# Kernel tuning notes

Hardware: AMD Instinct MI355X
Metric: run time of the kernel (lower is better)

Reference implementation:

```python
import jax, jax.numpy as jnp
import numpy as np

D = 128      # dim_hidden
L = 8        # topological levels (level 0 = primary inputs)
M = 32768    # nodes per level
N = L * M
G = 5        # gate types: maj/not/and/or/xor -> 5 param sets
F = 2        # fan-in per gate node


def setup_inputs() -> dict:
    key = jax.random.key(0)
    ks = jax.random.split(key, 18)
    p = lambda k, sh: jax.random.normal(k, sh, jnp.float32) * 0.05
    return {
        's': jax.random.normal(ks[0], (N, D), jnp.float32),
        't': jax.random.normal(ks[1], (N, D), jnp.float32),
        'gate': jax.random.randint(ks[2], (N,), 0, G, jnp.int32),
        'fanin': jax.random.randint(ks[3], (L - 1, M, F), 0, M, jnp.int32),
        'hs_W': p(ks[4], (2 * D, D)), 'hs_b': p(ks[5], (D,)),
        'aggr_W1': p(ks[6], (G, 2 * D, D)), 'aggr_b1': p(ks[7], (G, D)),
        'aggr_W2': p(ks[8], (G, D, D)), 'aggr_b2': p(ks[9], (G, D)),
        'aggr_W3': p(ks[10], (G, D, D)), 'aggr_b3': p(ks[11], (G, D)),
        'gru_Wi': p(ks[12], (G, D, 3 * D)), 'gru_Wh': p(ks[13], (G, D, 3 * D)),
        'gru_bi': p(ks[14], (G, 3 * D)), 'gru_bh': p(ks[15], (G, 3 * D)),
    }


def _forward(s, t, gate, fanin, hs_W, hs_b, aggr_W1, aggr_b1, aggr_W2, aggr_b2,
             aggr_W3, aggr_b3, gru_Wi, gru_Wh, gru_bi, gru_bh):
    hs = jnp.concatenate([s, t], -1) @ hs_W + hs_b          # [N,D]
    hf = jnp.zeros((N, D), hs.dtype)                        # functional state, zero-init
    for lvl in range(1, L):                                 # level-synchronous sweep
        lo = lvl * M
        g_l = gate[lo:lo + M]                               # [M] gate type of dst nodes
        oh = jax.nn.one_hot(g_l, G, dtype=hs.dtype)         # [M,G] gate selector
        src = (lvl - 1) * M + fanin[lvl - 1]                # [M,F] global fan-in indices
        src_state = jnp.concatenate([hs[src], hf[src]], -1)  # [M,F,2D] node_state gather
        # per-gate-type edge MLP (TFMlpAggr): 3-layer MLP on source states, sum over fan-in
        h1 = jax.nn.relu(jnp.einsum('mfc,gcd->gmfd', src_state, aggr_W1) + aggr_b1[:, None, None, :])
        h2 = jax.nn.relu(jnp.einsum('gmfd,gde->gmfe', h1, aggr_W2) + aggr_b2[:, None, None, :])
        m = jnp.einsum('gmfe,gek->gmfk', h2, aggr_W3) + aggr_b3[:, None, None, :]
        msg = jnp.einsum('gmd,mg->md', m.sum(axis=2), oh)   # [M,D] select own gate's aggr
        # per-gate-type GRU update of hf (torch GRU math, seq_len=1)
        h = hf[lo:lo + M]                                   # [M,D]
        gi = jnp.einsum('md,gdk->gmk', msg, gru_Wi) + gru_bi[:, None, :]  # [G,M,3D]
        gh = jnp.einsum('md,gdk->gmk', h, gru_Wh) + gru_bh[:, None, :]
        r = jax.nn.sigmoid(gi[..., :D] + gh[..., :D])
        z = jax.nn.sigmoid(gi[..., D:2 * D] + gh[..., D:2 * D])
        n = jnp.tanh(gi[..., 2 * D:] + r * gh[..., 2 * D:])
        h_new = jnp.einsum('gmd,mg->md', (1.0 - z) * n + z * h[None], oh)
        hf = hf.at[lo:lo + M].set(h_new)                    # scatter-write back
    return hs, hf


def reference(s, t, gate, fanin, hs_W, hs_b, aggr_W1, aggr_b1, aggr_W2, aggr_b2,
              aggr_W3, aggr_b3, gru_Wi, gru_Wh, gru_bi, gru_bh):
    return _forward(s, t, gate, fanin, hs_W, hs_b, aggr_W1, aggr_b1, aggr_W2,
                    aggr_b2, aggr_W3, aggr_b3, gru_Wi, gru_Wh, gru_bi, gru_bh)
```

## Files before the change

### kernel.cpp

```cpp
#include <hip/hip_runtime.h>
#include <hip/hip_bf16.h>

#define DD 128
#define LL 8
#define MM 32768
#define NN (LL*MM)
#define GG 5
#define FF 2
#define SORT_STRIDE 33408

typedef __attribute__((ext_vector_type(8))) short short8;
typedef __attribute__((ext_vector_type(4))) short short4v;
typedef __attribute__((ext_vector_type(4))) float f32x4;

#define MFMA16(a,b,c) __builtin_amdgcn_mfma_f32_16x16x32_bf16((a),(b),(c),0,0,0)

__device__ __forceinline__ short f2bf(float x){
  __hip_bfloat16 h = __float2bfloat16(x);
  return *reinterpret_cast<short*>(&h);
}

__device__ __forceinline__ short8 pack8(f32x4 a, f32x4 b){
  short8 r;
  r[0]=f2bf(a[0]); r[1]=f2bf(a[1]); r[2]=f2bf(a[2]); r[3]=f2bf(a[3]);
  r[4]=f2bf(b[0]); r[5]=f2bf(b[1]); r[6]=f2bf(b[2]); r[7]=f2bf(b[3]);
  return r;
}

__global__ void prep_kernel(const float* __restrict__ hs_W, const float* __restrict__ W1,
                            const float* __restrict__ W2, const float* __restrict__ W3,
                            const float* __restrict__ Wi,
                            short* __restrict__ hsWt, short* __restrict__ W1t,
                            short* __restrict__ W2t, short* __restrict__ W3t,
                            short* __restrict__ Wit, int* __restrict__ cntcur)
{
  if (blockIdx.x == 0 && threadIdx.x < 70) cntcur[threadIdx.x] = 0;
  int u = blockIdx.x*256 + threadIdx.x;
  const float* src; short* dst; int ldw;
  if (u < 4096){
    int i=u, ct=i>>9, kc=(i>>6)&7, lane=i&63;
    src = hs_W + (size_t)(kc*32 + 8*(lane>>4))*128 + ct*16 + (lane&15);
    dst = hsWt + (size_t)i*8; ldw=128;
  } else if (u < 24576){
    int v=u-4096, g=v>>12, i=v&4095, ct=i>>9, kc=(i>>6)&7, lane=i&63;
    src = W1 + (size_t)g*32768 + (size_t)(kc*32 + 8*(lane>>4))*128 + ct*16 + (lane&15);
    dst = W1t + (size_t)g*32768 + i*8; ldw=128;
  } else if (u < 34816){
    int v=u-24576, g=v>>11, i=v&2047, ct=i>>8, kc=(i>>6)&3, lane=i&63;
    src = W2 + (size_t)g*16384 + (size_t)(kc*32 + 8*(lane>>4))*128 + ct*16 + (lane&15);
    dst = W2t + (size_t)g*16384 + i*8; ldw=128;
  } else if (u < 45056){
    int v=u-34816, g=v>>11, i=v&2047, ct=i>>8, kc=(i>>6)&3, lane=i&63;
    src = W3 + (size_t)g*16384 + (size_t)(kc*32 + 8*(lane>>4))*128 + ct*16 + (lane&15);
    dst = W3t + (size_t)g*16384 + i*8; ldw=128;
  } else {
    int v=u-45056, g=v/6144, i=v%6144, ct=i>>8, kc=(i>>6)&3, lane=i&63;
    src = Wi + (size_t)g*49152 + (size_t)(kc*32 + 8*(lane>>4))*384 + ct*16 + (lane&15);
    dst = Wit + (size_t)g*49152 + i*8; ldw=384;
  }
  short8 o;
#pragma unroll
  for (int j=0;j<8;++j) o[j] = f2bf(src[(size_t)j*ldw]);
  *(short8*)dst = o;
}

__global__ void count_kernel(const int* __restrict__ gate, int* __restrict__ cnt){
  __shared__ int lc[GG];
  const int li = blockIdx.x >> 7;
  const int m  = ((blockIdx.x & 127) << 8) + threadIdx.x;
  if (threadIdx.x < GG) lc[threadIdx.x] = 0;
  __syncthreads();
  int g = gate[(li+1)*MM + m];
  atomicAdd(&lc[g], 1);
  __syncthreads();
  if (threadIdx.x < GG && lc[threadIdx.x] > 0)
    atomicAdd(&cnt[li*GG + threadIdx.x], lc[threadIdx.x]);
}

__global__ void offs_kernel(const int* __restrict__ cnt, int* __restrict__ off,
                            int* __restrict__ pend, int* __restrict__ sorted){
  __shared__ int se[35], sp[35];
  const int tid = threadIdx.x;
  if (tid < LL-1){
    int l = tid, o = 0;
    for (int g = 0; g < GG; ++g){
      off[l*GG+g] = o;
      int c = cnt[l*GG+g];
      pend[l*GG+g] = o + c;
      se[l*GG+g] = o + c;
      o += ((c + 31) >> 5) << 5;
      sp[l*GG+g] = o;
    }
  }
  __syncthreads();
  for (int b = 0; b < 35; ++b){
    int l = b / GG;
    for (int i = se[b] + tid; i < sp[b]; i += 256)
      sorted[l*SORT_STRIDE + i] = -1;
  }
}

__global__ void scatter_kernel(const int* __restrict__ gate, const int* __restrict__ off,
                               int* __restrict__ cur, int* __restrict__ sorted){
  __shared__ int lc[GG];
  __shared__ int base[GG];
  const int li = blockIdx.x >> 7;
  const int m  = ((blockIdx.x & 127) << 8) + threadIdx.x;
  if (threadIdx.x < GG) lc[threadIdx.x] = 0;
  __syncthreads();
  int g = gate[(li+1)*MM + m];
  int p = atomicAdd(&lc[g], 1);
  __syncthreads();
  if (threadIdx.x < GG)
    base[threadIdx.x] = atomicAdd(&cur[li*GG + threadIdx.x], lc[threadIdx.x]);
  __syncthreads();
  sorted[li*SORT_STRIDE + off[li*GG+g] + base[g] + p] = m;
}

__global__ __launch_bounds__(256,4) void hs_kernel(
    const float* __restrict__ s, const float* __restrict__ t,
    const short* __restrict__ Wt, const float* __restrict__ b,
    float* __restrict__ hs, short* __restrict__ hs_sh,
    float* __restrict__ hf, short* __restrict__ hf_sh)
{
  __shared__ __align__(16) short Xs[16384];
  const int tid=threadIdx.x, lane=tid&63, w=tid>>6;
  const int l15=lane&15, lq=lane>>4;
  const int row0 = blockIdx.x*64;

  {
    const int r = tid>>2, p = tid&3;
    const float* srow = s + (size_t)(row0+r)*DD;
    const float* trow = t + (size_t)(row0+r)*DD;
    const int rf = r>>4, rl = r&15;
#pragma unroll
    for (int i=0;i<8;++i){
      int u = p + 4*i;
      const float* pp = (u<16) ? (srow + 8*u) : (trow + 8*(u-16));
      short8 v = pack8(*(const f32x4*)pp, *(const f32x4*)(pp+4));
      *(short8*)(Xs + ((rf*8+(u>>2))*64 + (u&3)*16 + rl)*8) = v;
    }
  }

  if (row0 < MM){
    f32x4 zf4 = {0.f,0.f,0.f,0.f};
    short8 zs8 = {0,0,0,0,0,0,0,0};
    const size_t basei = (size_t)row0*DD;
#pragma unroll
    for (int i=tid; i<2048; i+=256) *(f32x4*)(hf + basei + i*4) = zf4;
#pragma unroll
    for (int i=tid; i<1024; i+=256) *(short8*)(hf_sh + basei + i*8) = zs8;
  }
  __syncthreads();

  f32x4 zf = {0.f,0.f,0.f,0.f};
  f32x4 acc[4][2];
#pragma unroll
  for (int rr=0;rr<4;++rr){ acc[rr][0]=zf; acc[rr][1]=zf; }

  const short* Ab = Wt + lane*8;
#pragma unroll
  for (int kc=0;kc<8;++kc){
    short8 a0 = *(const short8*)(Ab + (16*w + kc)*512);
    short8 a1 = *(const short8*)(Ab + (16*w + 8 + kc)*512);
#pragma unroll
    for (int rr=0;rr<4;++rr){
      short8 bx = *(const short8*)(Xs + ((rr*8 + kc)*64 + lane)*8);
      acc[rr][0] = MFMA16(a0, bx, acc[rr][0]);
      acc[rr][1] = MFMA16(a1, bx, acc[rr][1]);
    }
  }

  f32x4 bv0 = *(const f32x4*)(b + 32*w + 4*lq);
  f32x4 bv1 = *(const f32x4*)(b + 32*w + 16 + 4*lq);
#pragma unroll
  for (int rr=0;rr<4;++rr){
    int row = row0 + rr*16 + l15;
#pragma unroll
    for (int q=0;q<2;++q){
      f32x4 bv = q ? bv1 : bv0;
      int col = 32*w + 16*q + 4*lq;
      f32x4 o; short4v pk;
#pragma unroll
      for (int j=0;j<4;++j){ o[j] = acc[rr][q][j] + bv[j]; pk[j] = f2bf(o[j]); }
      *(f32x4*)(hs + (size_t)row*DD + col) = o;
      *(short4v*)(hs_sh + (size_t)row*DD + col) = pk;
    }
  }
}

__global__ __launch_bounds__(256,4) void level_kernel(
    int lvl, float* __restrict__ hfg,
    const short* __restrict__ hs_sh, short* __restrict__ hf_sh,
    const int* __restrict__ fanin,
    const short* __restrict__ W1t, const short* __restrict__ W2t,
    const short* __restrict__ W3t, const short* __restrict__ Wit,
    const float* __restrict__ b1, const float* __restrict__ b2,
    const float* __restrict__ b3, const float* __restrict__ bi,
    const float* __restrict__ bh,
    const int* __restrict__ off, const int* __restrict__ pend,
    const int* __restrict__ sorted)
{
  __shared__ __align__(16) short Xs[16384];
  __shared__ int nodebuf[32];
  __shared__ int srcbuf[64];
  __shared__ int ginfo;

  const int tid=threadIdx.x, lane=tid&63, w=tid>>6;
  const int l15=lane&15, lq=lane>>4;
  const int li = lvl-1;
  const int pos0 = blockIdx.x*32;

  if (tid==0){
    int g=-1;
    for (int q=0;q<GG;++q)
      if (pos0>=off[li*GG+q] && pos0<pend[li*GG+q]){ g=q; break; }
    ginfo=g;
  }
  if (tid<32) nodebuf[tid] = sorted[li*SORT_STRIDE + pos0 + tid];
  if (tid<64){
    int mg = sorted[li*SORT_STRIDE + pos0 + (tid>>1)];
    srcbuf[tid] = (mg>=0) ? li*MM + fanin[((size_t)li*MM+mg)*FF + (tid&1)] : 0;
  }
  __syncthreads();
  const int g = ginfo;
  if (g<0) return;

  {
    const int r = tid>>2, p = tid&3;
    const int src = srcbuf[r];
    const short* hsrow = hs_sh + (size_t)src*DD;
    const short* hfrow = hf_sh + (size_t)src*DD;
    const int rf = r>>4, rl = r&15;
#pragma unroll
    for (int i=0;i<8;++i){
      int u = p + 4*i;
      short8 v = *(const short8*)((u<16) ? (hsrow + 8*u) : (hfrow + 8*(u-16)));
      *(short8*)(Xs + ((rf*8+(u>>2))*64 + (u&3)*16 + rl)*8) = v;
    }
  }
  __syncthreads();

  f32x4 zf = {0.f,0.f,0.f,0.f};

  f32x4 acc[4][2];
#pragma unroll
  for (int rr=0;rr<4;++rr){ acc[rr][0]=zf; acc[rr][1]=zf; }
  const short* A1 = W1t + (size_t)g*32768 + lane*8;
#pragma unroll
  for (int kc=0;kc<8;++kc){
    short8 a0 = *(const short8*)(A1 + (16*w + kc)*512);
    short8 a1 = *(const short8*)(A1 + (16*w + 8 + kc)*512);
#pragma unroll
    for (int rr=0;rr<4;++rr){
      short8 bx = *(const short8*)(Xs + ((rr*8 + kc)*64 + lane)*8);
      acc[rr][0] = MFMA16(a0, bx, acc[rr][0]);
      acc[rr][1] = MFMA16(a1, bx, acc[rr][1]);
    }
  }
  __syncthreads();
  {
    f32x4 bv0 = *(const f32x4*)(b1 + g*DD + 32*w + 4*lq);
    f32x4 bv1 = *(const f32x4*)(b1 + g*DD + 32*w + 16 + 4*lq);
#pragma unroll
    for (int rr=0;rr<4;++rr){
#pragma unroll
      for (int q=0;q<2;++q){
        f32x4 bv = q ? bv1 : bv0;
        short4v pk;
#pragma unroll
        for (int j=0;j<4;++j) pk[j] = f2bf(fmaxf(acc[rr][q][j] + bv[j], 0.f));
        *(short4v*)(Xs + ((rr*4 + w)*64 + (2*q + (lq>>1))*16 + l15)*8 + 4*(lq&1)) = pk;
      }
    }
  }
  __syncthreads();

  f32x4 acc2[4][2];
#pragma unroll
  for (int rr=0;rr<4;++rr){ acc2[rr][0]=zf; acc2[rr][1]=zf; }
  const short* A2 = W2t + (size_t)g*16384 + lane*8;
#pragma unroll
  for (int kc=0;kc<4;++kc){
    short8 a0 = *(const short8*)(A2 + (8*w + kc)*512);
    short8 a1 = *(const short8*)(A2 + (8*w + 4 + kc)*512);
#pragma unroll
    for (int rr=0;rr<4;++rr){
      short8 bx = *(const short8*)(Xs + ((rr*4 + kc)*64 + lane)*8);
      acc2[rr][0] = MFMA16(a0, bx, acc2[rr][0]);
      acc2[rr][1] = MFMA16(a1, bx, acc2[rr][1]);
    }
  }
  {
    f32x4 bv0 = *(const f32x4*)(b2 + g*DD + 32*w + 4*lq);
    f32x4 bv1 = *(const f32x4*)(b2 + g*DD + 32*w + 16 + 4*lq);
#pragma unroll
    for (int rr=0;rr<4;++rr){
#pragma unroll
      for (int q=0;q<2;++q){
        f32x4 bv = q ? bv1 : bv0;
        short4v pk;
#pragma unroll
        for (int j=0;j<4;++j) pk[j] = f2bf(fmaxf(acc2[rr][q][j] + bv[j], 0.f));
        *(short4v*)(Xs + 8192 + ((rr*4 + w)*64 + (2*q + (lq>>1))*16 + l15)*8 + 4*(lq&1)) = pk;
      }
    }
  }
  __syncthreads();

  f32x4 acc3[4][2];
#pragma unroll
  for (int rr=0;rr<4;++rr){ acc3[rr][0]=zf; acc3[rr][1]=zf; }
  const short* A3 = W3t + (size_t)g*16384 + lane*8;
#pragma unroll
  for (int kc=0;kc<4;++kc){
    short8 a0 = *(const short8*)(A3 + (8*w + kc)*512);
    short8 a1 = *(const short8*)(A3 + (8*w + 4 + kc)*512);
#pragma unroll
    for (int rr=0;rr<4;++rr){
      short8 bx = *(const short8*)(Xs + 8192 + ((rr*4 + kc)*64 + lane)*8);
      acc3[rr][0] = MFMA16(a0, bx, acc3[rr][0]);
      acc3[rr][1] = MFMA16(a1, bx, acc3[rr][1]);
    }
  }
  {
    f32x4 bv0 = *(const f32x4*)(b3 + g*DD + 32*w + 4*lq);
    f32x4 bv1 = *(const f32x4*)(b3 + g*DD + 32*w + 16 + 4*lq);
#pragma unroll
    for (int rr=0;rr<4;++rr){
#pragma unroll
      for (int q=0;q<2;++q){
        f32x4 bv = q ? bv1 : bv0;
        f32x4 mv;
#pragma unroll
        for (int j=0;j<4;++j){
          float v = acc3[rr][q][j];
          mv[j] = v + __shfl_xor(v, 1) + 2.f*bv[j];
        }
        if ((l15 & 1) == 0){
          int n = rr*8 + (l15>>1);
          short4v pk;
#pragma unroll
          for (int j=0;j<4;++j) pk[j] = f2bf(mv[j]);
          *(short4v*)(Xs + (((n>>4)*4 + w)*64 + (2*q + (lq>>1))*16 + (n&15))*8 + 4*(lq&1)) = pk;
        }
      }
    }
  }
  __syncthreads();

  const short* AW = Wit + (size_t)g*49152 + lane*8;
  const int lo = lvl*MM;
#pragma unroll
  for (int q=0;q<2;++q){
    f32x4 gr[2], gz[2], gn[2];
    gr[0]=zf; gr[1]=zf; gz[0]=zf; gz[1]=zf; gn[0]=zf; gn[1]=zf;
#pragma unroll
    for (int kc=0;kc<4;++kc){
      int cti = ((2*w + q)*4 + kc)*512;
      short8 aR = *(const short8*)(AW + cti);
      short8 aZ = *(const short8*)(AW + 16384 + cti);
      short8 aN = *(const short8*)(AW + 32768 + cti);
#pragma unroll
      for (int rfm=0;rfm<2;++rfm){
        short8 bm = *(const short8*)(Xs + ((rfm*4 + kc)*64 + lane)*8);
        gr[rfm] = MFMA16(aR, bm, gr[rfm]);
        gz[rfm] = MFMA16(aZ, bm, gz[rfm]);
        gn[rfm] = MFMA16(aN, bm, gn[rfm]);
      }
    }
    int col = 32*w + 16*q + 4*lq;
    f32x4 biR = *(const f32x4*)(bi + g*384 + col);
    f32x4 biZ = *(const f32x4*)(bi + g*384 + 128 + col);
    f32x4 biN = *(const f32x4*)(bi + g*384 + 256 + col);
    f32x4 bhR = *(const f32x4*)(bh + g*384 + col);
    f32x4 bhZ = *(const f32x4*)(bh + g*384 + 128 + col);
    f32x4 bhN = *(const f32x4*)(bh + g*384 + 256 + col);
#pragma unroll
    for (int rfm=0;rfm<2;++rfm){
      int m = nodebuf[rfm*16 + l15];
      if (m < 0) continue;
      f32x4 o; short4v pk;
#pragma unroll
      for (int j=0;j<4;++j){
        float xr = gr[rfm][j] + biR[j] + bhR[j];
        float xz = gz[rfm][j] + biZ[j] + bhZ[j];
        float r_ = 1.f/(1.f + __expf(-xr));
        float z_ = 1.f/(1.f + __expf(-xz));
        float xn = gn[rfm][j] + biN[j] + r_*bhN[j];
        float n_ = 2.f/(1.f + __expf(-2.f*xn)) - 1.f;
        o[j] = (1.f - z_)*n_;
        pk[j] = f2bf(o[j]);
      }
      *(f32x4*)(hfg + (size_t)(lo + m)*DD + col) = o;
      *(short4v*)(hf_sh + (size_t)(lo + m)*DD + col) = pk;
    }
  }
}

extern "C" void kernel_launch(void* const* d_in, const int* in_sizes, int n_in,
                              void* d_out, int out_size, void* d_ws, size_t ws_size,
                              hipStream_t stream)
{
  const float* s    = (const float*)d_in[0];
  const float* t    = (const float*)d_in[1];
  const int*   gate = (const int*)d_in[2];
  const int*   fanin= (const int*)d_in[3];
  const float* hs_W = (const float*)d_in[4];
  const float* hs_b = (const float*)d_in[5];
  const float* W1   = (const float*)d_in[6];
  const float* b1   = (const float*)d_in[7];
  const float* W2   = (const float*)d_in[8];
  const float* b2   = (const float*)d_in[9];
  const float* W3   = (const float*)d_in[10];
  const float* b3   = (const float*)d_in[11];
  const float* Wi   = (const float*)d_in[12];
  const float* bi   = (const float*)d_in[14];
  const float* bh   = (const float*)d_in[15];

  float* hs = (float*)d_out;
  float* hf = hs + (size_t)NN*DD;

  int* cnt    = (int*)d_ws;
  int* cur    = cnt + 35;
  int* off    = cnt + 70;
  int* pendv  = cnt + 105;
  int* sorted = cnt + 256;

  short* wbase = (short*)((char*)d_ws + (1<<20));
  short* hsWt = wbase;
  short* W1t  = wbase + 32768;
  short* W2t  = wbase + 196608;
  short* W3t  = wbase + 278528;
  short* Wit  = wbase + 360448;

  short* hs_sh = (short*)((char*)d_ws + (size_t)(8<<20));
  short* hf_sh = hs_sh + (size_t)NN*DD;

  prep_kernel<<<296, 256, 0, stream>>>(hs_W, W1, W2, W3, Wi,
                                       hsWt, W1t, W2t, W3t, Wit, cnt);
  count_kernel<<<896, 256, 0, stream>>>(gate, cnt);
  offs_kernel<<<1, 256, 0, stream>>>(cnt, off, pendv, sorted);
  scatter_kernel<<<896, 256, 0, stream>>>(gate, off, cur, sorted);
  hs_kernel<<<NN/64, 256, 0, stream>>>(s, t, hsWt, hs_b, hs, hs_sh, hf, hf_sh);
  for (int lvl = 1; lvl < LL; ++lvl){
    level_kernel<<<SORT_STRIDE/32, 256, 0, stream>>>(lvl, hf,
        hs_sh, hf_sh, fanin, W1t, W2t, W3t, Wit,
        b1, b2, b3, bi, bh, off, pendv, sorted);
  }
}
```

Measured before the change: 405.0 us.

## Restructure MLP kernels so each wave owns rows and feeds MFMA directly from global

```diff
diff --git a/kernel.cpp b/kernel.cpp
--- a/kernel.cpp
+++ b/kernel.cpp
@@ -38,24 +38,24 @@
   int u = blockIdx.x*256 + threadIdx.x;
   const float* src; short* dst; int ldw;
   if (u < 4096){
-    int i=u, ct=i>>9, kc=(i>>6)&7, lane=i&63;
-    src = hs_W + (size_t)(kc*32 + 8*(lane>>4))*128 + ct*16 + (lane&15);
+    int i=u, ct=i>>9, kc=(i>>6)&7, ln=i&63;
+    src = hs_W + (size_t)(kc*32 + 8*(ln>>4))*128 + ct*16 + (ln&15);
     dst = hsWt + (size_t)i*8; ldw=128;
   } else if (u < 24576){
-    int v=u-4096, g=v>>12, i=v&4095, ct=i>>9, kc=(i>>6)&7, lane=i&63;
-    src = W1 + (size_t)g*32768 + (size_t)(kc*32 + 8*(lane>>4))*128 + ct*16 + (lane&15);
+    int v=u-4096, g=v>>12, i=v&4095, ct=i>>9, kc=(i>>6)&7, ln=i&63;
+    src = W1 + (size_t)g*32768 + (size_t)(kc*32 + 8*(ln>>4))*128 + ct*16 + (ln&15);
     dst = W1t + (size_t)g*32768 + i*8; ldw=128;
   } else if (u < 34816){
-    int v=u-24576, g=v>>11, i=v&2047, ct=i>>8, kc=(i>>6)&3, lane=i&63;
-    src = W2 + (size_t)g*16384 + (size_t)(kc*32 + 8*(lane>>4))*128 + ct*16 + (lane&15);
+    int v=u-24576, g=v>>11, i=v&2047, ct=i>>8, kc=(i>>6)&3, ln=i&63;
+    src = W2 + (size_t)g*16384 + (size_t)(kc*32 + 8*(ln>>4))*128 + ct*16 + (ln&15);
     dst = W2t + (size_t)g*16384 + i*8; ldw=128;
   } else if (u < 45056){
-    int v=u-34816, g=v>>11, i=v&2047, ct=i>>8, kc=(i>>6)&3, lane=i&63;
-    src = W3 + (size_t)g*16384 + (size_t)(kc*32 + 8*(lane>>4))*128 + ct*16 + (lane&15);
+    int v=u-34816, g=v>>11, i=v&2047, ct=i>>8, kc=(i>>6)&3, ln=i&63;
+    src = W3 + (size_t)g*16384 + (size_t)(kc*32 + 8*(ln>>4))*128 + ct*16 + (ln&15);
     dst = W3t + (size_t)g*16384 + i*8; ldw=128;
   } else {
-    int v=u-45056, g=v/6144, i=v%6144, ct=i>>8, kc=(i>>6)&3, lane=i&63;
-    src = Wi + (size_t)g*49152 + (size_t)(kc*32 + 8*(lane>>4))*384 + ct*16 + (lane&15);
+    int v=u-45056, g=v/6144, i=v%6144, ct=i>>8, kc=(i>>6)&3, ln=i&63;
+    src = Wi + (size_t)g*49152 + (size_t)(kc*32 + 8*(ln>>4))*384 + ct*16 + (ln&15);
     dst = Wit + (size_t)g*49152 + i*8; ldw=384;
   }
   short8 o;
@@ -78,7 +78,8 @@
 }
 
 __global__ void offs_kernel(const int* __restrict__ cnt, int* __restrict__ off,
-                            int* __restrict__ pend, int* __restrict__ sorted){
+                            int* __restrict__ pend, int* __restrict__ pad_end,
+                            int* __restrict__ sorted){
   __shared__ int se[35], sp[35];
   const int tid = threadIdx.x;
   if (tid < LL-1){
@@ -91,6 +92,7 @@
       o += ((c + 31) >> 5) << 5;
       sp[l*GG+g] = o;
     }
+    pad_end[l] = o;
   }
   __syncthreads();
   for (int b = 0; b < 35; ++b){
@@ -123,69 +125,45 @@
     float* __restrict__ hs, short* __restrict__ hs_sh,
     float* __restrict__ hf, short* __restrict__ hf_sh)
 {
-  __shared__ __align__(16) short Xs[16384];
   const int tid=threadIdx.x, lane=tid&63, w=tid>>6;
   const int l15=lane&15, lq=lane>>4;
   const int row0 = blockIdx.x*64;
-
-  {
-    const int r = tid>>2, p = tid&3;
-    const float* srow = s + (size_t)(row0+r)*DD;
-    const float* trow = t + (size_t)(row0+r)*DD;
-    const int rf = r>>4, rl = r&15;
-#pragma unroll
-    for (int i=0;i<8;++i){
-      int u = p + 4*i;
-      const float* pp = (u<16) ? (srow + 8*u) : (trow + 8*(u-16));
-      short8 v = pack8(*(const f32x4*)pp, *(const f32x4*)(pp+4));
-      *(short8*)(Xs + ((rf*8+(u>>2))*64 + (u&3)*16 + rl)*8) = v;
-    }
-  }
+  const int row = row0 + 16*w + l15;
 
   if (row0 < MM){
     f32x4 zf4 = {0.f,0.f,0.f,0.f};
     short8 zs8 = {0,0,0,0,0,0,0,0};
     const size_t basei = (size_t)row0*DD;
-#pragma unroll
     for (int i=tid; i<2048; i+=256) *(f32x4*)(hf + basei + i*4) = zf4;
-#pragma unroll
     for (int i=tid; i<1024; i+=256) *(short8*)(hf_sh + basei + i*8) = zs8;
   }
-  __syncthreads();
 
   f32x4 zf = {0.f,0.f,0.f,0.f};
-  f32x4 acc[4][2];
-#pragma unroll
-  for (int rr=0;rr<4;++rr){ acc[rr][0]=zf; acc[rr][1]=zf; }
-
+  f32x4 acc[8];
+#pragma unroll
+  for (int ct=0;ct<8;++ct) acc[ct] = zf;
+
+  const float* srow = s + (size_t)row*DD + 8*lq;
+  const float* trow = t + (size_t)row*DD + 8*lq;
   const short* Ab = Wt + lane*8;
 #pragma unroll
   for (int kc=0;kc<8;++kc){
-    short8 a0 = *(const short8*)(Ab + (16*w + kc)*512);
-    short8 a1 = *(const short8*)(Ab + (16*w + 8 + kc)*512);
-#pragma unroll
-    for (int rr=0;rr<4;++rr){
-      short8 bx = *(const short8*)(Xs + ((rr*8 + kc)*64 + lane)*8);
-      acc[rr][0] = MFMA16(a0, bx, acc[rr][0]);
-      acc[rr][1] = MFMA16(a1, bx, acc[rr][1]);
-    }
-  }
-
-  f32x4 bv0 = *(const f32x4*)(b + 32*w + 4*lq);
-  f32x4 bv1 = *(const f32x4*)(b + 32*w + 16 + 4*lq);
-#pragma unroll
-  for (int rr=0;rr<4;++rr){
-    int row = row0 + rr*16 + l15;
-#pragma unroll
-    for (int q=0;q<2;++q){
-      f32x4 bv = q ? bv1 : bv0;
-      int col = 32*w + 16*q + 4*lq;
-      f32x4 o; short4v pk;
-#pragma unroll
-      for (int j=0;j<4;++j){ o[j] = acc[rr][q][j] + bv[j]; pk[j] = f2bf(o[j]); }
-      *(f32x4*)(hs + (size_t)row*DD + col) = o;
-      *(short4v*)(hs_sh + (size_t)row*DD + col) = pk;
-    }
+    const float* p = (kc<4) ? (srow + kc*32) : (trow + (kc-4)*32);
+    short8 bx = pack8(*(const f32x4*)p, *(const f32x4*)(p+4));
+#pragma unroll
+    for (int ct=0;ct<8;++ct){
+      short8 a0 = *(const short8*)(Ab + (ct*8 + kc)*512);
+      acc[ct] = MFMA16(a0, bx, acc[ct]);
+    }
+  }
+#pragma unroll
+  for (int ct=0;ct<8;++ct){
+    f32x4 bv = *(const f32x4*)(b + ct*16 + 4*lq);
+    f32x4 o; short4v pk;
+#pragma unroll
+    for (int j=0;j<4;++j){ o[j] = acc[ct][j] + bv[j]; pk[j] = f2bf(o[j]); }
+    *(f32x4*)(hs + (size_t)row*DD + ct*16 + 4*lq) = o;
+    *(short4v*)(hs_sh + (size_t)row*DD + ct*16 + 4*lq) = pk;
   }
 }
 
@@ -199,152 +177,100 @@
     const float* __restrict__ b3, const float* __restrict__ bi,
     const float* __restrict__ bh,
     const int* __restrict__ off, const int* __restrict__ pend,
-    const int* __restrict__ sorted)
+    const int* __restrict__ pad_end, const int* __restrict__ sorted)
 {
-  __shared__ __align__(16) short Xs[16384];
-  __shared__ int nodebuf[32];
-  __shared__ int srcbuf[64];
-  __shared__ int ginfo;
+  __shared__ __align__(16) short bounce[4][16*136];
+  __shared__ __align__(16) short msgb[32*136];
 
   const int tid=threadIdx.x, lane=tid&63, w=tid>>6;
   const int l15=lane&15, lq=lane>>4;
   const int li = lvl-1;
   const int pos0 = blockIdx.x*32;
 
-  if (tid==0){
-    int g=-1;
-    for (int q=0;q<GG;++q)
-      if (pos0>=off[li*GG+q] && pos0<pend[li*GG+q]){ g=q; break; }
-    ginfo=g;
-  }
-  if (tid<32) nodebuf[tid] = sorted[li*SORT_STRIDE + pos0 + tid];
-  if (tid<64){
-    int mg = sorted[li*SORT_STRIDE + pos0 + (tid>>1)];
-    srcbuf[tid] = (mg>=0) ? li*MM + fanin[((size_t)li*MM+mg)*FF + (tid&1)] : 0;
-  }
-  __syncthreads();
-  const int g = ginfo;
-  if (g<0) return;
-
-  {
-    const int r = tid>>2, p = tid&3;
-    const int src = srcbuf[r];
-    const short* hsrow = hs_sh + (size_t)src*DD;
-    const short* hfrow = hf_sh + (size_t)src*DD;
-    const int rf = r>>4, rl = r&15;
-#pragma unroll
-    for (int i=0;i<8;++i){
-      int u = p + 4*i;
-      short8 v = *(const short8*)((u<16) ? (hsrow + 8*u) : (hfrow + 8*(u-16)));
-      *(short8*)(Xs + ((rf*8+(u>>2))*64 + (u&3)*16 + rl)*8) = v;
-    }
-  }
-  __syncthreads();
+  if (pos0 >= pad_end[li]) return;
+
+  int g = -1;
+#pragma unroll
+  for (int q=0;q<GG;++q)
+    if (pos0 >= off[li*GG+q] && pos0 < pend[li*GG+q]) g = q;
+  if (g < 0) return;
+
+  const int r = 16*w + l15;
+  const int mg = sorted[li*SORT_STRIDE + pos0 + (r>>1)];
+  const int src = (mg>=0) ? li*MM + fanin[((size_t)li*MM+mg)*FF + (r&1)] : 0;
+  const short* hsrow = hs_sh + (size_t)src*DD + 8*lq;
+  const short* hfrow = hf_sh + (size_t)src*DD + 8*lq;
 
   f32x4 zf = {0.f,0.f,0.f,0.f};
-
-  f32x4 acc[4][2];
-#pragma unroll
-  for (int rr=0;rr<4;++rr){ acc[rr][0]=zf; acc[rr][1]=zf; }
+  short* hb = bounce[w];
+
+  f32x4 acc[8];
+#pragma unroll
+  for (int ct=0;ct<8;++ct) acc[ct] = zf;
   const short* A1 = W1t + (size_t)g*32768 + lane*8;
 #pragma unroll
   for (int kc=0;kc<8;++kc){
-    short8 a0 = *(const short8*)(A1 + (16*w + kc)*512);
-    short8 a1 = *(const short8*)(A1 + (16*w + 8 + kc)*512);
-#pragma unroll
-    for (int rr=0;rr<4;++rr){
-      short8 bx = *(const short8*)(Xs + ((rr*8 + kc)*64 + lane)*8);
-      acc[rr][0] = MFMA16(a0, bx, acc[rr][0]);
-      acc[rr][1] = MFMA16(a1, bx, acc[rr][1]);
-    }
-  }
-  __syncthreads();
-  {
-    f32x4 bv0 = *(const f32x4*)(b1 + g*DD + 32*w + 4*lq);
-    f32x4 bv1 = *(const f32x4*)(b1 + g*DD + 32*w + 16 + 4*lq);
-#pragma unroll
-    for (int rr=0;rr<4;++rr){
-#pragma unroll
-      for (int q=0;q<2;++q){
-        f32x4 bv = q ? bv1 : bv0;
-        short4v pk;
-#pragma unroll
-        for (int j=0;j<4;++j) pk[j] = f2bf(fmaxf(acc[rr][q][j] + bv[j], 0.f));
-        *(short4v*)(Xs + ((rr*4 + w)*64 + (2*q + (lq>>1))*16 + l15)*8 + 4*(lq&1)) = pk;
-      }
-    }
-  }
-  __syncthreads();
-
-  f32x4 acc2[4][2];
-#pragma unroll
-  for (int rr=0;rr<4;++rr){ acc2[rr][0]=zf; acc2[rr][1]=zf; }
+    short8 bx = (kc<4) ? *(const short8*)(hsrow + kc*32)
+                       : *(const short8*)(hfrow + (kc-4)*32);
+#pragma unroll
+    for (int ct=0;ct<8;++ct)
+      acc[ct] = MFMA16(*(const short8*)(A1 + (ct*8 + kc)*512), bx, acc[ct]);
+  }
+#pragma unroll
+  for (int ct=0;ct<8;++ct){
+    f32x4 bv = *(const f32x4*)(b1 + g*DD + ct*16 + 4*lq);
+    short4v pk;
+#pragma unroll
+    for (int j=0;j<4;++j) pk[j] = f2bf(fmaxf(acc[ct][j] + bv[j], 0.f));
+    *(short4v*)(hb + l15*136 + ct*16 + 4*lq) = pk;
+  }
+
+  f32x4 acc2[8];
+#pragma unroll
+  for (int ct=0;ct<8;++ct) acc2[ct] = zf;
   const short* A2 = W2t + (size_t)g*16384 + lane*8;
 #pragma unroll
   for (int kc=0;kc<4;++kc){
-    short8 a0 = *(const short8*)(A2 + (8*w + kc)*512);
-    short8 a1 = *(const short8*)(A2 + (8*w + 4 + kc)*512);
-#pragma unroll
-    for (int rr=0;rr<4;++rr){
-      short8 bx = *(const short8*)(Xs + ((rr*4 + kc)*64 + lane)*8);
-      acc2[rr][0] = MFMA16(a0, bx, acc2[rr][0]);
-      acc2[rr][1] = MFMA16(a1, bx, acc2[rr][1]);
-    }
-  }
-  {
-    f32x4 bv0 = *(const f32x4*)(b2 + g*DD + 32*w + 4*lq);
-    f32x4 bv1 = *(const f32x4*)(b2 + g*DD + 32*w + 16 + 4*lq);
-#pragma unroll
-    for (int rr=0;rr<4;++rr){
-#pragma unroll
-      for (int q=0;q<2;++q){
-        f32x4 bv = q ? bv1 : bv0;
-        short4v pk;
-#pragma unroll
-        for (int j=0;j<4;++j) pk[j] = f2bf(fmaxf(acc2[rr][q][j] + bv[j], 0.f));
-        *(short4v*)(Xs + 8192 + ((rr*4 + w)*64 + (2*q + (lq>>1))*16 + l15)*8 + 4*(lq&1)) = pk;
-      }
-    }
-  }
-  __syncthreads();
-
-  f32x4 acc3[4][2];
-#pragma unroll
-  for (int rr=0;rr<4;++rr){ acc3[rr][0]=zf; acc3[rr][1]=zf; }
+    short8 bx = *(const short8*)(hb + l15*136 + kc*32 + 8*lq);
+#pragma unroll
+    for (int ct=0;ct<8;++ct)
+      acc2[ct] = MFMA16(*(const short8*)(A2 + (ct*4 + kc)*512), bx, acc2[ct]);
+  }
+#pragma unroll
+  for (int ct=0;ct<8;++ct){
+    f32x4 bv = *(const f32x4*)(b2 + g*DD + ct*16 + 4*lq);
+    short4v pk;
+#pragma unroll
+    for (int j=0;j<4;++j) pk[j] = f2bf(fmaxf(acc2[ct][j] + bv[j], 0.f));
+    *(short4v*)(hb + l15*136 + ct*16 + 4*lq) = pk;
+  }
+
+  f32x4 acc3[8];
+#pragma unroll
+  for (int ct=0;ct<8;++ct) acc3[ct] = zf;
   const short* A3 = W3t + (size_t)g*16384 + lane*8;
 #pragma unroll
   for (int kc=0;kc<4;++kc){
-    short8 a0 = *(const short8*)(A3 + (8*w + kc)*512);
-    short8 a1 = *(const short8*)(A3 + (8*w + 4 + kc)*512);
-#pragma unroll
-    for (int rr=0;rr<4;++rr){
-      short8 bx = *(const short8*)(Xs + 8192 + ((rr*4 + kc)*64 + lane)*8);
-      acc3[rr][0] = MFMA16(a0, bx, acc3[rr][0]);
-      acc3[rr][1] = MFMA16(a1, bx, acc3[rr][1]);
-    }
-  }
-  {
-    f32x4 bv0 = *(const f32x4*)(b3 + g*DD + 32*w + 4*lq);
-    f32x4 bv1 = *(const f32x4*)(b3 + g*DD + 32*w + 16 + 4*lq);
-#pragma unroll
-    for (int rr=0;rr<4;++rr){
-#pragma unroll
-      for (int q=0;q<2;++q){
-        f32x4 bv = q ? bv1 : bv0;
-        f32x4 mv;
-#pragma unroll
-        for (int j=0;j<4;++j){
-          float v = acc3[rr][q][j];
-          mv[j] = v + __shfl_xor(v, 1) + 2.f*bv[j];
-        }
-        if ((l15 & 1) == 0){
-          int n = rr*8 + (l15>>1);
-          short4v pk;
-#pragma unroll
-          for (int j=0;j<4;++j) pk[j] = f2bf(mv[j]);
-          *(short4v*)(Xs + (((n>>4)*4 + w)*64 + (2*q + (lq>>1))*16 + (n&15))*8 + 4*(lq&1)) = pk;
-        }
-      }
+    short8 bx = *(const short8*)(hb + l15*136 + kc*32 + 8*lq);
+#pragma unroll
+    for (int ct=0;ct<8;++ct)
+      acc3[ct] = MFMA16(*(const short8*)(A3 + (ct*4 + kc)*512), bx, acc3[ct]);
+  }
+#pragma unroll
+  for (int ct=0;ct<8;++ct){
+    f32x4 bv = *(const f32x4*)(b3 + g*DD + ct*16 + 4*lq);
+    f32x4 mv;
+#pragma unroll
+    for (int j=0;j<4;++j){
+      float v = acc3[ct][j];
+      mv[j] = v + __shfl_xor(v, 1) + 2.f*bv[j];
+    }
+    if ((l15 & 1) == 0){
+      int n = 8*w + (l15>>1);
+      short4v pk;
+#pragma unroll
+      for (int j=0;j<4;++j) pk[j] = f2bf(mv[j]);
+      *(short4v*)(msgb + n*136 + ct*16 + 4*lq) = pk;
     }
   }
   __syncthreads();
@@ -363,7 +289,7 @@
       short8 aN = *(const short8*)(AW + 32768 + cti);
 #pragma unroll
       for (int rfm=0;rfm<2;++rfm){
-        short8 bm = *(const short8*)(Xs + ((rfm*4 + kc)*64 + lane)*8);
+        short8 bm = *(const short8*)(msgb + (rfm*16 + l15)*136 + kc*32 + 8*lq);
         gr[rfm] = MFMA16(aR, bm, gr[rfm]);
         gz[rfm] = MFMA16(aZ, bm, gz[rfm]);
         gn[rfm] = MFMA16(aN, bm, gn[rfm]);
@@ -378,7 +304,7 @@
     f32x4 bhN = *(const f32x4*)(bh + g*384 + 256 + col);
 #pragma unroll
     for (int rfm=0;rfm<2;++rfm){
-      int m = nodebuf[rfm*16 + l15];
+      int m = sorted[li*SORT_STRIDE + pos0 + rfm*16 + l15];
       if (m < 0) continue;
       f32x4 o; short4v pk;
 #pragma unroll
@@ -421,11 +347,12 @@
   float* hs = (float*)d_out;
   float* hf = hs + (size_t)NN*DD;
 
-  int* cnt    = (int*)d_ws;
-  int* cur    = cnt + 35;
-  int* off    = cnt + 70;
-  int* pendv  = cnt + 105;
-  int* sorted = cnt + 256;
+  int* cnt     = (int*)d_ws;
+  int* cur     = cnt + 35;
+  int* off     = cnt + 70;
+  int* pendv   = cnt + 105;
+  int* pad_end = cnt + 140;
+  int* sorted  = cnt + 256;
 
   short* wbase = (short*)((char*)d_ws + (1<<20));
   short* hsWt = wbase;
@@ -440,12 +367,12 @@
   prep_kernel<<<296, 256, 0, stream>>>(hs_W, W1, W2, W3, Wi,
                                        hsWt, W1t, W2t, W3t, Wit, cnt);
   count_kernel<<<896, 256, 0, stream>>>(gate, cnt);
-  offs_kernel<<<1, 256, 0, stream>>>(cnt, off, pendv, sorted);
+  offs_kernel<<<1, 256, 0, stream>>>(cnt, off, pendv, pad_end, sorted);
   scatter_kernel<<<896, 256, 0, stream>>>(gate, off, cur, sorted);
   hs_kernel<<<NN/64, 256, 0, stream>>>(s, t, hsWt, hs_b, hs, hs_sh, hf, hf_sh);
   for (int lvl = 1; lvl < LL; ++lvl){
     level_kernel<<<SORT_STRIDE/32, 256, 0, stream>>>(lvl, hf,
         hs_sh, hf_sh, fanin, W1t, W2t, W3t, Wit,
-        b1, b2, b3, bi, bh, off, pendv, sorted);
-  }
-}
+        b1, b2, b3, bi, bh, off, pendv, pad_end, sorted);
+  }
+}
```

New measurement: 702.5 us. 1.73x slower.
